# Performance work log

Hardware: AMD Instinct MI355X
Metric: run time of the kernel (lower is better)

## Reference

```python
import jax, jax.numpy as jnp
import numpy as np

EPS = 1e-7  # K.epsilon()
B, S, W1, W2, D = 256, 4, 64, 128, 300
HID = 4


def setup_inputs() -> dict:
    key = jax.random.key(0)
    k1, k2, k3, k4, k5, k6, k7 = jax.random.split(key, 7)
    return {
        "tuple1": jax.random.normal(k1, (B, S, W1, D), dtype=jnp.float32),
        "tuple2": jax.random.normal(k2, (B, S, W2, D), dtype=jnp.float32),
        "mask1": jax.random.randint(k3, (B, S, W1), 0, 2, dtype=jnp.int32),
        "mask2": jax.random.randint(k4, (B, S, W2), 0, 2, dtype=jnp.int32),
        "threshold": jax.random.normal(k5, (), dtype=jnp.float32),
        "W_hidden": jax.random.normal(k6, (S, HID), dtype=jnp.float32) * 0.5,
        "W_score": jax.random.normal(k7, (HID, 1), dtype=jnp.float32) * 0.5,
    }


def reference(tuple1, tuple2, mask1, mask2, threshold, W_hidden, W_score):
    # Pairwise dot-product similarity between every tuple1 word and tuple2 word per slot.
    sim = jnp.einsum("bswd,bsvd->bswv", tuple1, tuple2)  # (B, S, W1, W2)
    m1 = mask1.astype(jnp.float32)
    m2 = mask2.astype(jnp.float32)
    overlap = (sim >= threshold).astype(jnp.float32)
    overlap = overlap * m1[:, :, :, None] * m2[:, :, None, :]
    slot_overlap = jnp.sum(overlap, axis=(2, 3))  # (B, S)
    count1 = jnp.sum(m1, axis=2)  # (B, S)
    divisor = jnp.where(count1 == 0, EPS, count1)
    normalized = slot_overlap / divisor  # (B, S)
    h = jnp.tanh(normalized @ W_hidden)  # (B, HID)
    return jax.nn.sigmoid(h @ W_score)  # (B, 1)
```

## Files before the change

### kernel.cpp

```cpp
#include <hip/hip_runtime.h>
#include <math.h>

#define B_   256
#define S_   4
#define W1_  64
#define W2_  128
#define D_   300
#define HID_ 4
#define KT   60
#define NKT  5
#define PADK 64

__global__ __launch_bounds__(256) void sim_count_kernel(
    const float* __restrict__ t1, const float* __restrict__ t2,
    const int* __restrict__ m1, const int* __restrict__ m2,
    const float* __restrict__ thr_p, float* __restrict__ norm_out)
{
    __shared__ float As[W1_ * PADK];
    __shared__ float Bs[W2_ * PADK];
    __shared__ int widx[W1_];
    __shared__ int vidx[W2_];
    __shared__ int cntA, cntB, cntOv;

    const int bs  = blockIdx.x;
    const int tid = threadIdx.x;
    const float thr = *thr_p;

    if (tid == 0) { cntA = 0; cntB = 0; cntOv = 0; }
    __syncthreads();

    if (tid < W1_) {
        if (m1[bs * W1_ + tid] != 0) {
            int p = atomicAdd(&cntA, 1);
            widx[p] = tid;
        }
    } else if (tid < W1_ + W2_) {
        int v = tid - W1_;
        if (m2[bs * W2_ + v] != 0) {
            int p = atomicAdd(&cntB, 1);
            vidx[p] = v;
        }
    }
    __syncthreads();

    const int nA = cntA, nB = cntB;
    const int Ra = (nA + 3) >> 2;
    const int Cb = (nB + 7) >> 3;
    const int Ta = Ra * Cb;

    int tr = 0, tc = 0;
    const bool active = (tid < Ta);
    if (active) { tr = tid / Cb; tc = tid - tr * Cb; }
    const int swa = tr & 7;
    const int swb = tc & 7;

    float acc[4][8];
    #pragma unroll
    for (int i = 0; i < 4; ++i)
        #pragma unroll
        for (int j = 0; j < 8; ++j) acc[i][j] = 0.f;

    const float* t1b = t1 + (size_t)bs * W1_ * D_;
    const float* t2b = t2 + (size_t)bs * W2_ * D_;

    for (int kt = 0; kt < NKT; ++kt) {
        const int k0 = kt * KT;
        for (int idx = tid; idx < nA * (KT / 4); idx += 256) {
            int a = idx / (KT / 4);
            int f = idx - a * (KT / 4);
            const float4 val = *reinterpret_cast<const float4*>(
                t1b + (size_t)widx[a] * D_ + k0 + 4 * f);
            *reinterpret_cast<float4*>(
                &As[a * PADK + 4 * (f ^ ((a >> 2) & 7))]) = val;
        }
        for (int idx = tid; idx < nB * (KT / 4); idx += 256) {
            int v = idx / (KT / 4);
            int f = idx - v * (KT / 4);
            const float4 val = *reinterpret_cast<const float4*>(
                t2b + (size_t)vidx[v] * D_ + k0 + 4 * f);
            *reinterpret_cast<float4*>(
                &Bs[v * PADK + 4 * (f ^ ((v >> 3) & 7))]) = val;
        }
        __syncthreads();

        if (active) {
            #pragma unroll
            for (int g = 0; g < KT / 4; ++g) {
                float4 av[4];
                float4 bv[8];
                #pragma unroll
                for (int i = 0; i < 4; ++i)
                    av[i] = *reinterpret_cast<const float4*>(
                        &As[(4 * tr + i) * PADK + 4 * (g ^ swa)]);
                #pragma unroll
                for (int j = 0; j < 8; ++j)
                    bv[j] = *reinterpret_cast<const float4*>(
                        &Bs[(8 * tc + j) * PADK + 4 * (g ^ swb)]);
                #pragma unroll
                for (int i = 0; i < 4; ++i)
                    #pragma unroll
                    for (int j = 0; j < 8; ++j) {
                        acc[i][j] = fmaf(av[i].x, bv[j].x, acc[i][j]);
                        acc[i][j] = fmaf(av[i].y, bv[j].y, acc[i][j]);
                        acc[i][j] = fmaf(av[i].z, bv[j].z, acc[i][j]);
                        acc[i][j] = fmaf(av[i].w, bv[j].w, acc[i][j]);
                    }
            }
        }
        __syncthreads();
    }

    int lc = 0;
    if (active) {
        const int ilim = min(nA - 4 * tr, 4);
        const int jlim = min(nB - 8 * tc, 8);
        #pragma unroll
        for (int i = 0; i < 4; ++i)
            #pragma unroll
            for (int j = 0; j < 8; ++j)
                lc += ((i < ilim) & (j < jlim) & (acc[i][j] >= thr)) ? 1 : 0;
    }
    #pragma unroll
    for (int o = 32; o > 0; o >>= 1) lc += __shfl_down(lc, o);
    if ((tid & 63) == 0 && lc != 0) atomicAdd(&cntOv, lc);
    __syncthreads();

    if (tid == 0) {
        float divisor = (nA == 0) ? 1e-7f : (float)nA;
        norm_out[bs] = (float)cntOv / divisor;
    }
}

__global__ __launch_bounds__(256) void head_kernel(
    const float* __restrict__ norm,
    const float* __restrict__ Wh,
    const float* __restrict__ Ws,
    float* __restrict__ out)
{
    int b = blockIdx.x * blockDim.x + threadIdx.x;
    if (b >= B_) return;
    float4 n = *reinterpret_cast<const float4*>(norm + b * 4);
    float score = 0.f;
    #pragma unroll
    for (int j = 0; j < HID_; ++j) {
        float h = n.x * Wh[0 * HID_ + j] + n.y * Wh[1 * HID_ + j]
                + n.z * Wh[2 * HID_ + j] + n.w * Wh[3 * HID_ + j];
        h = tanhf(h);
        score += h * Ws[j];
    }
    out[b] = 1.f / (1.f + expf(-score));
}

extern "C" void kernel_launch(void* const* d_in, const int* in_sizes, int n_in,
                              void* d_out, int out_size, void* d_ws, size_t ws_size,
                              hipStream_t stream)
{
    const float* t1  = (const float*)d_in[0];
    const float* t2  = (const float*)d_in[1];
    const int*   m1  = (const int*)d_in[2];
    const int*   m2  = (const int*)d_in[3];
    const float* thr = (const float*)d_in[4];
    const float* Wh  = (const float*)d_in[5];
    const float* Ws  = (const float*)d_in[6];
    float* out  = (float*)d_out;
    float* norm = (float*)d_ws;

    sim_count_kernel<<<B_ * S_, 256, 0, stream>>>(t1, t2, m1, m2, thr, norm);
    head_kernel<<<1, 256, 0, stream>>>(norm, Wh, Ws, out);
}
```

Before: 313.0 us.

## Split K reduction across the four wavefronts with an LDS partial-sum reduce

Each of the four 64-thread wavefronts now computes the same 4x8 output tiles over a quarter of the K groups in every staged slice. The partial sums are then reduced through shared memory, reusing the Bs buffer, before thresholding. Previously the output tile count was typically about 64, so usually only one wavefront per block did the FMA work. Tile counts above 64 are now processed in chunks of 64. Each chunk restages all inputs from global memory, and the inner group loop no longer has compile-time bounds, so it is no longer fully unrolled.

Result: slower. 320.0 us (+2.2%).

```diff
diff --git a/kernel.cpp b/kernel.cpp
--- a/kernel.cpp
+++ b/kernel.cpp
@@ -9,6 +9,7 @@
 #define HID_ 4
 #define KT   60
 #define NKT  5
+#define NG   15
 #define PADK 64
 
 __global__ __launch_bounds__(256) void sim_count_kernel(
@@ -30,16 +31,10 @@
     __syncthreads();
 
     if (tid < W1_) {
-        if (m1[bs * W1_ + tid] != 0) {
-            int p = atomicAdd(&cntA, 1);
-            widx[p] = tid;
-        }
+        if (m1[bs * W1_ + tid] != 0) { int p = atomicAdd(&cntA, 1); widx[p] = tid; }
     } else if (tid < W1_ + W2_) {
         int v = tid - W1_;
-        if (m2[bs * W2_ + v] != 0) {
-            int p = atomicAdd(&cntB, 1);
-            vidx[p] = v;
-        }
+        if (m2[bs * W2_ + v] != 0) { int p = atomicAdd(&cntB, 1); vidx[p] = v; }
     }
     __syncthreads();
 
@@ -47,83 +42,101 @@
     const int Ra = (nA + 3) >> 2;
     const int Cb = (nB + 7) >> 3;
     const int Ta = Ra * Cb;
+    const int nChunks = (Ta + 63) >> 6;
 
-    int tr = 0, tc = 0;
-    const bool active = (tid < Ta);
-    if (active) { tr = tid / Cb; tc = tid - tr * Cb; }
-    const int swa = tr & 7;
-    const int swb = tc & 7;
+    const int sh = tid >> 6;
+    const int tl = tid & 63;
+    const int gs = (NG * sh) >> 2;
+    const int ge = (NG * (sh + 1)) >> 2;
 
-    float acc[4][8];
-    #pragma unroll
-    for (int i = 0; i < 4; ++i)
-        #pragma unroll
-        for (int j = 0; j < 8; ++j) acc[i][j] = 0.f;
+    float* Ps = Bs;
 
     const float* t1b = t1 + (size_t)bs * W1_ * D_;
     const float* t2b = t2 + (size_t)bs * W2_ * D_;
 
-    for (int kt = 0; kt < NKT; ++kt) {
-        const int k0 = kt * KT;
-        for (int idx = tid; idx < nA * (KT / 4); idx += 256) {
-            int a = idx / (KT / 4);
-            int f = idx - a * (KT / 4);
-            const float4 val = *reinterpret_cast<const float4*>(
-                t1b + (size_t)widx[a] * D_ + k0 + 4 * f);
-            *reinterpret_cast<float4*>(
-                &As[a * PADK + 4 * (f ^ ((a >> 2) & 7))]) = val;
+    for (int chunk = 0; chunk < nChunks; ++chunk) {
+        const int T = chunk * 64 + tl;
+        const bool active = (T < Ta);
+        int tr = 0, tc = 0;
+        if (active) { tr = T / Cb; tc = T - tr * Cb; }
+        const int swa = tr & 7;
+        const int swb = tc & 7;
+
+        float acc[4][8];
+        #pragma unroll
+        for (int i = 0; i < 4; ++i)
+            #pragma unroll
+            for (int j = 0; j < 8; ++j) acc[i][j] = 0.f;
+
+        for (int kt = 0; kt < NKT; ++kt) {
+            const int k0 = kt * KT;
+            for (int idx = tid; idx < nA * NG; idx += 256) {
+                int a = idx / NG;
+                int f = idx - a * NG;
+                const float4 val = *reinterpret_cast<const float4*>(
+                    t1b + (size_t)widx[a] * D_ + k0 + 4 * f);
+                *reinterpret_cast<float4*>(
+                    &As[a * PADK + 4 * (f ^ ((a >> 2) & 7))]) = val;
+            }
+            for (int idx = tid; idx < nB * NG; idx += 256) {
+                int v = idx / NG;
+                int f = idx - v * NG;
+                const float4 val = *reinterpret_cast<const float4*>(
+                    t2b + (size_t)vidx[v] * D_ + k0 + 4 * f);
+                *reinterpret_cast<float4*>(
+                    &Bs[v * PADK + 4 * (f ^ ((v >> 3) & 7))]) = val;
+            }
+            __syncthreads();
+
+            if (active) {
+                for (int g = gs; g < ge; ++g) {
+                    float4 av[4];
+                    float4 bv[8];
+                    #pragma unroll
+                    for (int i = 0; i < 4; ++i)
+                        av[i] = *reinterpret_cast<const float4*>(
+                            &As[(4 * tr + i) * PADK + 4 * (g ^ swa)]);
+                    #pragma unroll
+                    for (int j = 0; j < 8; ++j)
+                        bv[j] = *reinterpret_cast<const float4*>(
+                            &Bs[(8 * tc + j) * PADK + 4 * (g ^ swb)]);
+                    #pragma unroll
+                    for (int i = 0; i < 4; ++i)
+                        #pragma unroll
+                        for (int j = 0; j < 8; ++j) {
+                            acc[i][j] = fmaf(av[i].x, bv[j].x, acc[i][j]);
+                            acc[i][j] = fmaf(av[i].y, bv[j].y, acc[i][j]);
+                            acc[i][j] = fmaf(av[i].z, bv[j].z, acc[i][j]);
+                            acc[i][j] = fmaf(av[i].w, bv[j].w, acc[i][j]);
+                        }
+                }
+            }
+            __syncthreads();
         }
-        for (int idx = tid; idx < nB * (KT / 4); idx += 256) {
-            int v = idx / (KT / 4);
-            int f = idx - v * (KT / 4);
-            const float4 val = *reinterpret_cast<const float4*>(
-                t2b + (size_t)vidx[v] * D_ + k0 + 4 * f);
-            *reinterpret_cast<float4*>(
-                &Bs[v * PADK + 4 * (f ^ ((v >> 3) & 7))]) = val;
-        }
-        __syncthreads();
 
-        if (active) {
-            #pragma unroll
-            for (int g = 0; g < KT / 4; ++g) {
-                float4 av[4];
-                float4 bv[8];
-                #pragma unroll
-                for (int i = 0; i < 4; ++i)
-                    av[i] = *reinterpret_cast<const float4*>(
-                        &As[(4 * tr + i) * PADK + 4 * (g ^ swa)]);
-                #pragma unroll
-                for (int j = 0; j < 8; ++j)
-                    bv[j] = *reinterpret_cast<const float4*>(
-                        &Bs[(8 * tc + j) * PADK + 4 * (g ^ swb)]);
-                #pragma unroll
-                for (int i = 0; i < 4; ++i)
-                    #pragma unroll
-                    for (int j = 0; j < 8; ++j) {
-                        acc[i][j] = fmaf(av[i].x, bv[j].x, acc[i][j]);
-                        acc[i][j] = fmaf(av[i].y, bv[j].y, acc[i][j]);
-                        acc[i][j] = fmaf(av[i].z, bv[j].z, acc[i][j]);
-                        acc[i][j] = fmaf(av[i].w, bv[j].w, acc[i][j]);
-                    }
-            }
-        }
-        __syncthreads();
-    }
-
-    int lc = 0;
-    if (active) {
-        const int ilim = min(nA - 4 * tr, 4);
-        const int jlim = min(nB - 8 * tc, 8);
         #pragma unroll
         for (int i = 0; i < 4; ++i)
             #pragma unroll
             for (int j = 0; j < 8; ++j)
-                lc += ((i < ilim) & (j < jlim) & (acc[i][j] >= thr)) ? 1 : 0;
+                Ps[(i * 8 + j) * 256 + sh * 64 + tl] = acc[i][j];
+        __syncthreads();
+
+        int lc = 0;
+        if (active) {
+            #pragma unroll
+            for (int j = 0; j < 8; ++j) {
+                const int o = sh * 8 + j;
+                float sum = Ps[o * 256 + 0 * 64 + tl] + Ps[o * 256 + 1 * 64 + tl]
+                          + Ps[o * 256 + 2 * 64 + tl] + Ps[o * 256 + 3 * 64 + tl];
+                const bool valid = (4 * tr + sh < nA) && (8 * tc + j < nB);
+                lc += (valid && (sum >= thr)) ? 1 : 0;
+            }
+        }
+        #pragma unroll
+        for (int o = 32; o > 0; o >>= 1) lc += __shfl_down(lc, o);
+        if ((tid & 63) == 0 && lc != 0) atomicAdd(&cntOv, lc);
+        __syncthreads();
     }
-    #pragma unroll
-    for (int o = 32; o > 0; o >>= 1) lc += __shfl_down(lc, o);
-    if ((tid & 63) == 0 && lc != 0) atomicAdd(&cntOv, lc);
-    __syncthreads();
 
     if (tid == 0) {
         float divisor = (nA == 0) ? 1e-7f : (float)nA;
```

## Compute similarity GEMM with split-bf16 MFMA and register-prefetched K tiles

Applied to the files above, without the earlier changes.

Replaces the scalar FP32 FMA dot-product tiles with bf16 MFMA 16x16x32 instructions. Each FP32 value is split into high and low bf16 halves, and three MFMAs per tile recover near-FP32 accuracy. The next K tile is prefetched into registers while the current one is being computed. Masking moves from compacting the valid rows to computing every row and masking the counts afterwards. This trades skipping masked rows and exact FP32 rounding for matrix-core throughput and overlap of loads with compute. Similarity values close to the threshold may compare differently than in FP32.

After: 297.8 us. -4.9%, faster.

```diff
diff --git a/kernel.cpp b/kernel.cpp
--- a/kernel.cpp
+++ b/kernel.cpp
@@ -1,133 +1,164 @@
 #include <hip/hip_runtime.h>
 #include <math.h>
 
-#define B_   256
-#define S_   4
-#define W1_  64
-#define W2_  128
-#define D_   300
-#define HID_ 4
-#define KT   60
-#define NKT  5
-#define PADK 64
-
-__global__ __launch_bounds__(256) void sim_count_kernel(
+#define B_    256
+#define S_    4
+#define W1_   64
+#define W2_   128
+#define D_    300
+#define HID_  4
+#define KTILE 64
+#define NT    5
+
+typedef short          s16x8 __attribute__((ext_vector_type(8)));
+typedef float          fx4   __attribute__((ext_vector_type(4)));
+typedef unsigned short us4   __attribute__((ext_vector_type(4)));
+
+#define AHI_OFF 0
+#define ALO_OFF 8192
+#define BHI_OFF 16384
+#define BLO_OFF 32768
+#define LDS_BYTES 49152
+
+__device__ __forceinline__ void split_bf16(float x, unsigned short& h, unsigned short& l) {
+    union { float f; unsigned u; } c; c.f = x;
+    unsigned uh = c.u + 0x7FFFu + ((c.u >> 16) & 1u);
+    h = (unsigned short)(uh >> 16);
+    union { unsigned u; float f; } hb; hb.u = ((unsigned)h) << 16;
+    float r = x - hb.f;
+    union { float f; unsigned u; } cr; cr.f = r;
+    unsigned ul = cr.u + 0x7FFFu + ((cr.u >> 16) & 1u);
+    l = (unsigned short)(ul >> 16);
+}
+
+__global__ __launch_bounds__(256, 3) void sim_count_mfma(
     const float* __restrict__ t1, const float* __restrict__ t2,
     const int* __restrict__ m1, const int* __restrict__ m2,
     const float* __restrict__ thr_p, float* __restrict__ norm_out)
 {
-    __shared__ float As[W1_ * PADK];
-    __shared__ float Bs[W2_ * PADK];
-    __shared__ int widx[W1_];
-    __shared__ int vidx[W2_];
-    __shared__ int cntA, cntB, cntOv;
+    __shared__ unsigned char lds[LDS_BYTES];
+    __shared__ int m1s[W1_];
+    __shared__ int m2s[W2_];
+    __shared__ int sh_nA, sh_cnt;
 
     const int bs  = blockIdx.x;
     const int tid = threadIdx.x;
     const float thr = *thr_p;
 
-    if (tid == 0) { cntA = 0; cntB = 0; cntOv = 0; }
-    __syncthreads();
-
-    if (tid < W1_) {
-        if (m1[bs * W1_ + tid] != 0) {
-            int p = atomicAdd(&cntA, 1);
-            widx[p] = tid;
-        }
-    } else if (tid < W1_ + W2_) {
-        int v = tid - W1_;
-        if (m2[bs * W2_ + v] != 0) {
-            int p = atomicAdd(&cntB, 1);
-            vidx[p] = v;
-        }
-    }
-    __syncthreads();
-
-    const int nA = cntA, nB = cntB;
-    const int Ra = (nA + 3) >> 2;
-    const int Cb = (nB + 7) >> 3;
-    const int Ta = Ra * Cb;
-
-    int tr = 0, tc = 0;
-    const bool active = (tid < Ta);
-    if (active) { tr = tid / Cb; tc = tid - tr * Cb; }
-    const int swa = tr & 7;
-    const int swb = tc & 7;
-
-    float acc[4][8];
-    #pragma unroll
-    for (int i = 0; i < 4; ++i)
-        #pragma unroll
-        for (int j = 0; j < 8; ++j) acc[i][j] = 0.f;
-
     const float* t1b = t1 + (size_t)bs * W1_ * D_;
     const float* t2b = t2 + (size_t)bs * W2_ * D_;
 
-    for (int kt = 0; kt < NKT; ++kt) {
-        const int k0 = kt * KT;
-        for (int idx = tid; idx < nA * (KT / 4); idx += 256) {
-            int a = idx / (KT / 4);
-            int f = idx - a * (KT / 4);
-            const float4 val = *reinterpret_cast<const float4*>(
-                t1b + (size_t)widx[a] * D_ + k0 + 4 * f);
-            *reinterpret_cast<float4*>(
-                &As[a * PADK + 4 * (f ^ ((a >> 2) & 7))]) = val;
+    if (tid == 0) sh_cnt = 0;
+    if (tid < W1_) {
+        int m = m1[bs * W1_ + tid];
+        m1s[tid] = m;
+        unsigned long long bal = __ballot(m != 0);
+        if (tid == 0) sh_nA = __popcll(bal);
+    } else if (tid < W1_ + W2_) {
+        m2s[tid - W1_] = m2[bs * W2_ + (tid - W1_)];
+    }
+
+    fx4 stg[12];
+
+    auto stage_issue = [&](int t) {
+        #pragma unroll
+        for (int p = 0; p < 12; ++p) {
+            const int idx = tid + (p << 8);
+            const bool isA = (idx < 1024);
+            const int sub = isA ? idx : idx - 1024;
+            const int row = sub >> 4;
+            const int g   = sub & 15;
+            const float* src = (isA ? t1b : t2b) + row * D_ + t * KTILE + 4 * g;
+            fx4 v; v[0] = 0.f; v[1] = 0.f; v[2] = 0.f; v[3] = 0.f;
+            if ((t < 4) | (g <= 10)) v = *(const fx4*)src;
+            stg[p] = v;
         }
-        for (int idx = tid; idx < nB * (KT / 4); idx += 256) {
-            int v = idx / (KT / 4);
-            int f = idx - v * (KT / 4);
-            const float4 val = *reinterpret_cast<const float4*>(
-                t2b + (size_t)vidx[v] * D_ + k0 + 4 * f);
-            *reinterpret_cast<float4*>(
-                &Bs[v * PADK + 4 * (f ^ ((v >> 3) & 7))]) = val;
+    };
+    auto cvt_write = [&]() {
+        #pragma unroll
+        for (int p = 0; p < 12; ++p) {
+            const int idx = tid + (p << 8);
+            const bool isA = (idx < 1024);
+            const int sub = isA ? idx : idx - 1024;
+            const int row = sub >> 4;
+            const int g   = sub & 15;
+            us4 hv, lv;
+            #pragma unroll
+            for (int e = 0; e < 4; ++e) {
+                unsigned short h, l;
+                split_bf16(stg[p][e], h, l);
+                hv[e] = h; lv[e] = l;
+            }
+            const int off = (g * 8) ^ ((row & 7) << 4);
+            unsigned char* ph = lds + (isA ? AHI_OFF : BHI_OFF) + row * 128 + off;
+            unsigned char* pl = lds + (isA ? ALO_OFF : BLO_OFF) + row * 128 + off;
+            *(us4*)ph = hv;
+            *(us4*)pl = lv;
         }
-        __syncthreads();
-
-        if (active) {
+    };
+
+    const int l  = tid & 63;
+    const int w  = tid >> 6;
+    const int lr = l & 15;
+    const int lg = l >> 4;
+    const int arow  = (w << 4) + lr;
+    const int abase = arow * 128;
+    const int asw   = (arow & 7) << 4;
+
+    fx4 acc[8];
+    {
+        fx4 z; z[0] = 0.f; z[1] = 0.f; z[2] = 0.f; z[3] = 0.f;
+        #pragma unroll
+        for (int ct = 0; ct < 8; ++ct) acc[ct] = z;
+    }
+
+    stage_issue(0);
+    cvt_write();
+    __syncthreads();
+
+    for (int t = 0; t < NT; ++t) {
+        if (t + 1 < NT) stage_issue(t + 1);
+        #pragma unroll
+        for (int ks = 0; ks < 2; ++ks) {
+            const int koff = ks * 64 + lg * 16;
+            const s16x8 ah = *(const s16x8*)(lds + AHI_OFF + abase + (koff ^ asw));
+            const s16x8 al = *(const s16x8*)(lds + ALO_OFF + abase + (koff ^ asw));
             #pragma unroll
-            for (int g = 0; g < KT / 4; ++g) {
-                float4 av[4];
-                float4 bv[8];
-                #pragma unroll
-                for (int i = 0; i < 4; ++i)
-                    av[i] = *reinterpret_cast<const float4*>(
-                        &As[(4 * tr + i) * PADK + 4 * (g ^ swa)]);
-                #pragma unroll
-                for (int j = 0; j < 8; ++j)
-                    bv[j] = *reinterpret_cast<const float4*>(
-                        &Bs[(8 * tc + j) * PADK + 4 * (g ^ swb)]);
-                #pragma unroll
-                for (int i = 0; i < 4; ++i)
-                    #pragma unroll
-                    for (int j = 0; j < 8; ++j) {
-                        acc[i][j] = fmaf(av[i].x, bv[j].x, acc[i][j]);
-                        acc[i][j] = fmaf(av[i].y, bv[j].y, acc[i][j]);
-                        acc[i][j] = fmaf(av[i].z, bv[j].z, acc[i][j]);
-                        acc[i][j] = fmaf(av[i].w, bv[j].w, acc[i][j]);
-                    }
+            for (int ct = 0; ct < 8; ++ct) {
+                const int v    = (ct << 4) + lr;
+                const int boff = koff ^ ((v & 7) << 4);
+                const s16x8 bh = *(const s16x8*)(lds + BHI_OFF + v * 128 + boff);
+                const s16x8 bl = *(const s16x8*)(lds + BLO_OFF + v * 128 + boff);
+                acc[ct] = __builtin_amdgcn_mfma_f32_16x16x32_bf16(ah, bh, acc[ct], 0, 0, 0);
+                acc[ct] = __builtin_amdgcn_mfma_f32_16x16x32_bf16(ah, bl, acc[ct], 0, 0, 0);
+                acc[ct] = __builtin_amdgcn_mfma_f32_16x16x32_bf16(al, bh, acc[ct], 0, 0, 0);
             }
         }
         __syncthreads();
-    }
+        if (t + 1 < NT) { cvt_write(); __syncthreads(); }
+    }
+
+    int am[4];
+    #pragma unroll
+    for (int r = 0; r < 4; ++r) am[r] = m1s[(w << 4) + lg * 4 + r];
 
     int lc = 0;
-    if (active) {
-        const int ilim = min(nA - 4 * tr, 4);
-        const int jlim = min(nB - 8 * tc, 8);
-        #pragma unroll
-        for (int i = 0; i < 4; ++i)
-            #pragma unroll
-            for (int j = 0; j < 8; ++j)
-                lc += ((i < ilim) & (j < jlim) & (acc[i][j] >= thr)) ? 1 : 0;
+    #pragma unroll
+    for (int ct = 0; ct < 8; ++ct) {
+        const int bm = m2s[(ct << 4) + lr];
+        #pragma unroll
+        for (int r = 0; r < 4; ++r)
+            lc += ((acc[ct][r] >= thr) & (am[r] != 0) & (bm != 0)) ? 1 : 0;
     }
     #pragma unroll
     for (int o = 32; o > 0; o >>= 1) lc += __shfl_down(lc, o);
-    if ((tid & 63) == 0 && lc != 0) atomicAdd(&cntOv, lc);
+    if ((tid & 63) == 0 && lc) atomicAdd(&sh_cnt, lc);
     __syncthreads();
 
     if (tid == 0) {
-        float divisor = (nA == 0) ? 1e-7f : (float)nA;
-        norm_out[bs] = (float)cntOv / divisor;
+        const int nA = sh_nA;
+        const float divisor = (nA == 0) ? 1e-7f : (float)nA;
+        norm_out[bs] = (float)sh_cnt / divisor;
     }
 }
 
@@ -139,12 +170,12 @@
 {
     int b = blockIdx.x * blockDim.x + threadIdx.x;
     if (b >= B_) return;
-    float4 n = *reinterpret_cast<const float4*>(norm + b * 4);
+    fx4 n = *reinterpret_cast<const fx4*>(norm + b * 4);
     float score = 0.f;
     #pragma unroll
     for (int j = 0; j < HID_; ++j) {
-        float h = n.x * Wh[0 * HID_ + j] + n.y * Wh[1 * HID_ + j]
-                + n.z * Wh[2 * HID_ + j] + n.w * Wh[3 * HID_ + j];
+        float h = n[0] * Wh[0 * HID_ + j] + n[1] * Wh[1 * HID_ + j]
+                + n[2] * Wh[2 * HID_ + j] + n[3] * Wh[3 * HID_ + j];
         h = tanhf(h);
         score += h * Ws[j];
     }
@@ -165,6 +196,6 @@
     float* out  = (float*)d_out;
     float* norm = (float*)d_ws;
 
-    sim_count_kernel<<<B_ * S_, 256, 0, stream>>>(t1, t2, m1, m2, thr, norm);
+    sim_count_mfma<<<B_ * S_, 256, 0, stream>>>(t1, t2, m1, m2, thr, norm);
     head_kernel<<<1, 256, 0, stream>>>(norm, Wh, Ws, out);
 }
```
